# Kernel optimization log

Hardware: AMD Instinct MI355X
Metric: run time of the kernel (lower is better)

The kernel has to match this reference:

```python
import jax, jax.numpy as jnp
import numpy as np

T, B, IN, H, L, C = 512, 4096, 12, 32, 10, 4


def setup_inputs() -> dict:
    key = jax.random.key(0)
    ks = jax.random.split(key, 12)
    s = 1.0 / np.sqrt(H)  # PyTorch GRU init scale ~ U(-1/sqrt(H), 1/sqrt(H))
    return {
        "x": jax.random.normal(ks[0], (T, B, IN), jnp.float32),
        "W_ih0": jax.random.normal(ks[1], (3 * H, IN), jnp.float32) * s,
        "W_hh0": jax.random.normal(ks[2], (3 * H, H), jnp.float32) * s,
        "b_ih0": jax.random.normal(ks[3], (3 * H,), jnp.float32) * s,
        "b_hh0": jax.random.normal(ks[4], (3 * H,), jnp.float32) * s,
        "W_ih": jax.random.normal(ks[5], (L - 1, 3 * H, H), jnp.float32) * s,
        "W_hh": jax.random.normal(ks[6], (L - 1, 3 * H, H), jnp.float32) * s,
        "b_ih": jax.random.normal(ks[7], (L - 1, 3 * H), jnp.float32) * s,
        "b_hh": jax.random.normal(ks[8], (L - 1, 3 * H), jnp.float32) * s,
        "fc_W": jax.random.normal(ks[9], (C, H), jnp.float32) * s,
        "fc_b": jax.random.normal(ks[10], (C,), jnp.float32) * s,
        "lengths": jax.random.randint(ks[11], (B,), 1, T + 1, jnp.int32),
    }


def gru_cell(x_t, h, Wi, Wh, bi, bh):
    # PyTorch GRU cell math
    gi = x_t @ Wi.T + bi          # [B, 3H]
    gh = h @ Wh.T + bh            # [B, 3H]
    i_r, i_z, i_n = jnp.split(gi, 3, axis=-1)
    h_r, h_z, h_n = jnp.split(gh, 3, axis=-1)
    r = jax.nn.sigmoid(i_r + h_r)
    z = jax.nn.sigmoid(i_z + h_z)
    n = jnp.tanh(i_n + r * h_n)
    return (1.0 - z) * n + z * h


def reference(x, W_ih0, W_hh0, b_ih0, b_hh0, W_ih, W_hh, b_ih, b_hh, fc_W, fc_b, lengths):
    Bn = x.shape[1]
    h0 = jnp.zeros((L, Bn, H), x.dtype)

    def step(h, x_t):
        hs = []
        inp = x_t
        for l in range(L):
            if l == 0:
                hl = gru_cell(inp, h[0], W_ih0, W_hh0, b_ih0, b_hh0)
            else:
                hl = gru_cell(inp, h[l], W_ih[l - 1], W_hh[l - 1], b_ih[l - 1], b_hh[l - 1])
            hs.append(hl)
            inp = hl
        return jnp.stack(hs), inp  # carry all-layer hidden, emit top-layer output

    _, outs = jax.lax.scan(step, h0, x)  # [T, B, H]
    idx = jnp.maximum(lengths, 1) - 1    # last valid timestep per sequence
    last = outs[idx, jnp.arange(Bn)]     # [B, H]
    logits = last @ fc_W.T + fc_b        # [B, C]
    return jax.nn.log_softmax(logits, axis=1)
```

## Files before the change

### kernel.cpp

```cpp
#include <hip/hip_runtime.h>
#include <math.h>

#define TT 512
#define BB 4096
#define IN_DIM 12
#define HH 32
#define LL 10
#define CC 4
#define NTH (LL * 64)

typedef _Float16 half8 __attribute__((ext_vector_type(8)));
typedef _Float16 half4 __attribute__((ext_vector_type(4)));
typedef float f32x4 __attribute__((ext_vector_type(4)));
typedef float f32x2 __attribute__((ext_vector_type(2)));

#define LOG2E 1.44269504088896340736f

#define H_HI 0
#define H_LO (LL * 8 * 512)
#define X_HI (H_LO + LL * 2 * 512)
#define LDS16_TOT (X_HI + 4 * 512)

#define MFMA_(A, B, C) C = __builtin_amdgcn_mfma_f32_16x16x32_f16(A, B, C, 0, 0, 0)

__global__ __launch_bounds__(NTH, 2)
void gru_fused_mfma(const float* __restrict__ x,
                    const float* __restrict__ Wih0,
                    const float* __restrict__ Whh0,
                    const float* __restrict__ bih0,
                    const float* __restrict__ bhh0,
                    const float* __restrict__ Wih,
                    const float* __restrict__ Whh,
                    const float* __restrict__ bih,
                    const float* __restrict__ bhh,
                    const int*   __restrict__ lengths,
                    float*       __restrict__ last)
{
    __shared__ __align__(16) _Float16 lds16[LDS16_TOT];
    __shared__ int flagS[LL];
    __shared__ int rflagS[LL];

    const int tid  = threadIdx.x;
    const int w    = tid >> 6;
    const int lane = tid & 63;
    const int bi16 = lane & 15;
    const int quad = lane >> 4;
    const int bg   = blockIdx.x;

    {
        float4 z4 = make_float4(0.f, 0.f, 0.f, 0.f);
        float4* p = (float4*)lds16;
        for (int i = tid; i < LDS16_TOT / 8; i += NTH) p[i] = z4;
    }
    if (lane == 0) { flagS[w] = -1; rflagS[w] = -1; }
    __syncthreads();

    const float *Wi, *Wh, *bivec, *bhvec;
    int wistride;
    if (w == 0) { Wi = Wih0; Wh = Whh0; bivec = bih0; bhvec = bhh0; wistride = IN_DIM; }
    else {
        Wi = Wih + (size_t)(w - 1) * 96 * HH;
        Wh = Whh + (size_t)(w - 1) * 96 * HH;
        bivec = bih + (size_t)(w - 1) * 96;
        bhvec = bhh + (size_t)(w - 1) * 96;
        wistride = HH;
    }

    const int frow[12] = {0, 0, 16, 16, 32, 32, 48, 48, 64, 80, 64, 80};
    const int fchk[12] = {0, 1, 0, 1, 0, 1, 0, 1, 0, 0, 1, 1};
    half8 Whi[12], Wlo[6];
#pragma unroll
    for (int f = 0; f < 12; f++) {
        const float sc = (f < 8) ? -LOG2E : 2.0f * LOG2E;
        int row = frow[f] + bi16;
        const float* src; int kin;
        if (fchk[f] == 0) { src = Wi + (size_t)row * wistride; kin = wistride; }
        else              { src = Wh + (size_t)row * HH;       kin = HH; }
        int wloidx = (f < 8) ? (f >> 1) : (f - 6);
#pragma unroll
        for (int kk = 0; kk < 8; kk++) {
            int k = quad * 8 + kk;
            float v = (k < kin) ? src[k] * sc : 0.0f;
            _Float16 h = (_Float16)v;
            Whi[f][kk] = h;
            if (fchk[f] == 1) Wlo[wloidx][kk] = (_Float16)(v - (float)h);
        }
    }

    f32x4 biasreg[8];
#pragma unroll
    for (int ct = 0; ct < 8; ct++) {
        int g = ct >> 1, jt = ct & 1;
#pragma unroll
        for (int r = 0; r < 4; r++) {
            int j = jt * 16 + quad * 4 + r;
            float v;
            if      (g == 0) v = -(bivec[j]      + bhvec[j])      * LOG2E;
            else if (g == 1) v = -(bivec[32 + j] + bhvec[32 + j]) * LOG2E;
            else if (g == 2) v = bivec[64 + j] * (2.0f * LOG2E);
            else             v = bhvec[64 + j] * (2.0f * LOG2E);
            biasreg[ct][r] = v;
        }
    }

    int capT = -1;
    if (w == LL - 1) {
        int len = lengths[bg * 16 + bi16];
        capT = ((len < 1) ? 1 : len) - 1;
    }

    const int laneoff = lane * 8;
    const int inbase  = (w == 0) ? X_HI : (H_HI + (w - 1) * 4096);
    const int inmask  = (w == 0) ? 3 : 7;
    const int ownhi   = H_HI + w * 4096;
    const int ownlo   = H_LO + w * 1024;
    const int wibase  = (quad >> 1) * 128 + bi16 * 8 + (quad & 1) * 4;

    const int xbb = lane / 3, xkg = lane - xbb * 3;
    const int xq   = (xkg == 2) ? 1 : 0;
    const int xoff = (xkg == 1) ? 4 : 0;
    const int xidx = xq * 128 + xbb * 8 + xoff;
    const bool xlane = (w == 0) && (lane < 48);

    auto stage_x = [&](const float4& xl, int t) {
        half4 h4;
        h4[0] = (_Float16)xl.x; h4[1] = (_Float16)xl.y;
        h4[2] = (_Float16)xl.z; h4[3] = (_Float16)xl.w;
        *(half4*)(lds16 + X_HI + ((t & 3) << 9) + xidx) = h4;
    };

    if (xlane) {
        float4 x0 = *(const float4*)(x + (size_t)bg * 192 + lane * 4);
        float4 x1 = *(const float4*)(x + (size_t)BB * IN_DIM + (size_t)bg * 192 + lane * 4);
        stage_x(x0, 0);
        stage_x(x1, 1);
    }

    f32x2 hprev[4];
#pragma unroll
    for (int i = 0; i < 4; i++) { hprev[i][0] = 0.0f; hprev[i][1] = 0.0f; }

    __syncthreads();

    auto substep = [&](int t) {
        half8 bxh = *(const half8*)(lds16 + inbase + ((t & inmask) << 9) + laneoff);
        half8 bhh = *(const half8*)(lds16 + ownhi + (((t + 7) & 7) << 9) + laneoff);
        half8 bhl = *(const half8*)(lds16 + ownlo + (((t + 1) & 1) << 9) + laneoff);

        f32x4 acc[8];

#pragma unroll
        for (int ct = 0; ct < 4; ct++) {
            acc[ct] = __builtin_amdgcn_mfma_f32_16x16x32_f16(
                          Whi[ct * 2 + 0], bxh, biasreg[ct], 0, 0, 0);
            MFMA_(Whi[ct * 2 + 1], bhh, acc[ct]);
            MFMA_(Whi[ct * 2 + 1], bhl, acc[ct]);
            MFMA_(Wlo[ct],         bhh, acc[ct]);
        }
#pragma unroll
        for (int jt = 0; jt < 2; jt++) {
            acc[4 + jt] = __builtin_amdgcn_mfma_f32_16x16x32_f16(
                              Whi[8 + jt], bxh, biasreg[4 + jt], 0, 0, 0);
            acc[6 + jt] = __builtin_amdgcn_mfma_f32_16x16x32_f16(
                              Whi[10 + jt], bhh, biasreg[6 + jt], 0, 0, 0);
            MFMA_(Whi[10 + jt], bhl, acc[6 + jt]);
            MFMA_(Wlo[4 + jt],  bhh, acc[6 + jt]);
        }

#pragma unroll
        for (int jt = 0; jt < 2; jt++) {
            half4 h4, l4;
            float hv[4];
#pragma unroll
            for (int pr = 0; pr < 2; pr++) {
                f32x2 R2, Z2, I2, H2;
                R2[0] = acc[0 + jt][2 * pr]; R2[1] = acc[0 + jt][2 * pr + 1];
                Z2[0] = acc[2 + jt][2 * pr]; Z2[1] = acc[2 + jt][2 * pr + 1];
                I2[0] = acc[4 + jt][2 * pr]; I2[1] = acc[4 + jt][2 * pr + 1];
                H2[0] = acc[6 + jt][2 * pr]; H2[1] = acc[6 + jt][2 * pr + 1];
                f32x2 av, bv;
                av[0] = __builtin_amdgcn_exp2f(R2[0]);
                av[1] = __builtin_amdgcn_exp2f(R2[1]);
                bv[0] = __builtin_amdgcn_exp2f(Z2[0]);
                bv[1] = __builtin_amdgcn_exp2f(Z2[1]);
                av = av + 1.0f;
                bv = bv + 1.0f;
                f32x2 pv = av * bv;
                float q  = __builtin_amdgcn_rcpf(pv[0] * pv[1]);
                f32x2 qs; qs[0] = q * pv[1]; qs[1] = q * pv[0];
                f32x2 rv = qs * bv;
                f32x2 zv = qs * av;
                f32x2 na = __builtin_elementwise_fma(rv, H2, I2);
                f32x2 ea;
                ea[0] = __builtin_amdgcn_exp2f(na[0]);
                ea[1] = __builtin_amdgcn_exp2f(na[1]);
                f32x2 dv = ea + 1.0f;
                float qn = __builtin_amdgcn_rcpf(dv[0] * dv[1]);
                f32x2 qv; qv[0] = qn * dv[1]; qv[1] = qn * dv[0];
                f32x2 m2; m2[0] = -2.0f; m2[1] = -2.0f;
                f32x2 o1; o1[0] = 1.0f;  o1[1] = 1.0f;
                f32x2 nv = __builtin_elementwise_fma(m2, qv, o1);
                f32x2 hp = hprev[jt * 2 + pr];
                f32x2 hn = __builtin_elementwise_fma(zv, hp - nv, nv);
                hprev[jt * 2 + pr] = hn;
                _Float16 hh0 = (_Float16)hn[0], hh1 = (_Float16)hn[1];
                f32x2 hi32; hi32[0] = (float)hh0; hi32[1] = (float)hh1;
                f32x2 lo2 = hn - hi32;
                h4[2 * pr]     = hh0; h4[2 * pr + 1] = hh1;
                l4[2 * pr]     = (_Float16)lo2[0];
                l4[2 * pr + 1] = (_Float16)lo2[1];
                hv[2 * pr]     = hn[0];
                hv[2 * pr + 1] = hn[1];
            }
            int wi = jt * 256 + wibase;
            *(half4*)(lds16 + ownhi + ((t & 7) << 9) + wi) = h4;
            *(half4*)(lds16 + ownlo + ((t & 1) << 9) + wi) = l4;
            if (w == LL - 1 && t == capT) {
                float4 o = make_float4(hv[0], hv[1], hv[2], hv[3]);
                *(float4*)(last + (size_t)(bg * 16 + bi16) * HH + jt * 16 + quad * 4) = o;
            }
        }
    };

    for (int t = 0; t < TT; t += 2) {
        if (w > 0) {
            while (__hip_atomic_load(&flagS[w - 1], __ATOMIC_ACQUIRE,
                                     __HIP_MEMORY_SCOPE_WORKGROUP) < t + 1)
                __builtin_amdgcn_s_sleep(1);
        }
        if (w < LL - 1) {
            while (__hip_atomic_load(&rflagS[w], __ATOMIC_ACQUIRE,
                                     __HIP_MEMORY_SCOPE_WORKGROUP) < t - 7)
                __builtin_amdgcn_s_sleep(1);
        }

        float4 xa0, xa1;
        bool dl0 = false, dl1 = false;
        if (xlane) {
            if (t + 2 < TT) {
                xa0 = *(const float4*)(x + (size_t)(t + 2) * BB * IN_DIM +
                                       (size_t)bg * 192 + lane * 4);
                dl0 = true;
            }
            if (t + 3 < TT) {
                xa1 = *(const float4*)(x + (size_t)(t + 3) * BB * IN_DIM +
                                       (size_t)bg * 192 + lane * 4);
                dl1 = true;
            }
        }

        substep(t);
        substep(t + 1);

        if (dl0) stage_x(xa0, t + 2);
        if (dl1) stage_x(xa1, t + 3);

        if (lane == 0) {
            if (w < LL - 1)
                __hip_atomic_store(&flagS[w], t + 1, __ATOMIC_RELEASE,
                                   __HIP_MEMORY_SCOPE_WORKGROUP);
            if (w > 0)
                __hip_atomic_store(&rflagS[w - 1], t + 1, __ATOMIC_RELEASE,
                                   __HIP_MEMORY_SCOPE_WORKGROUP);
        }
    }
}

__global__ __launch_bounds__(256)
void fc_head(const float* __restrict__ last,
             const float* __restrict__ fcW,
             const float* __restrict__ fcb,
             float* __restrict__ out)
{
    int b = blockIdx.x * blockDim.x + threadIdx.x;
    if (b >= BB) return;
    float lg[CC];
#pragma unroll
    for (int c = 0; c < CC; c++) lg[c] = fcb[c];
#pragma unroll
    for (int j = 0; j < HH; j++) {
        float h = last[(size_t)b * HH + j];
#pragma unroll
        for (int c = 0; c < CC; c++) lg[c] = fmaf(fcW[c * HH + j], h, lg[c]);
    }
    float m = lg[0];
#pragma unroll
    for (int c = 1; c < CC; c++) m = fmaxf(m, lg[c]);
    float s = 0.0f;
#pragma unroll
    for (int c = 0; c < CC; c++) s += __expf(lg[c] - m);
    float lse = m + logf(s);
#pragma unroll
    for (int c = 0; c < CC; c++) out[(size_t)b * CC + c] = lg[c] - lse;
}

extern "C" void kernel_launch(void* const* d_in, const int* in_sizes, int n_in,
                              void* d_out, int out_size, void* d_ws, size_t ws_size,
                              hipStream_t stream)
{
    const float* x    = (const float*)d_in[0];
    const float* Wih0 = (const float*)d_in[1];
    const float* Whh0 = (const float*)d_in[2];
    const float* bih0 = (const float*)d_in[3];
    const float* bhh0 = (const float*)d_in[4];
    const float* Wih  = (const float*)d_in[5];
    const float* Whh  = (const float*)d_in[6];
    const float* bih  = (const float*)d_in[7];
    const float* bhh  = (const float*)d_in[8];
    const float* fcW  = (const float*)d_in[9];
    const float* fcb  = (const float*)d_in[10];
    const int*   lens = (const int*)d_in[11];
    float* out = (float*)d_out;

    float* last = (float*)d_ws;

    gru_fused_mfma<<<dim3(BB / 16), dim3(NTH), 0, stream>>>(
        x, Wih0, Whh0, bih0, bhh0, Wih, Whh, bih, bhh, lens, last);

    fc_head<<<dim3(BB / 256), dim3(256), 0, stream>>>(last, fcW, fcb, out);
}
```

Baseline: 908.7 us.

## Split last two GRU layers across two waves each to shorten pipeline critical path

Raises the block from 10 to 12 waves. Layers 8 and 9 are now each handled by two waves, and each wave of a pair computes one half (jt tile) of the hidden units. The sibling waves sync every substep through a new sibF flag array, and the forward and backward flag dependencies are rewired for the split layers. The intent is to speed up the slowest tail stages of the layer wavefront pipeline, at the cost of more waves per block (which can lower occupancy) and extra per-substep spin-waits.

```diff
diff --git a/kernel.cpp b/kernel.cpp
--- a/kernel.cpp
+++ b/kernel.cpp
@@ -7,7 +7,7 @@
 #define HH 32
 #define LL 10
 #define CC 4
-#define NTH (LL * 64)
+#define NTH 768
 
 typedef _Float16 half8 __attribute__((ext_vector_type(8)));
 typedef _Float16 half4 __attribute__((ext_vector_type(4)));
@@ -37,8 +37,9 @@
                     float*       __restrict__ last)
 {
     __shared__ __align__(16) _Float16 lds16[LDS16_TOT];
-    __shared__ int flagS[LL];
-    __shared__ int rflagS[LL];
+    __shared__ int flagS[12];
+    __shared__ int rflagS[12];
+    __shared__ int sibF[4];
 
     const int tid  = threadIdx.x;
     const int w    = tid >> 6;
@@ -47,22 +48,27 @@
     const int quad = lane >> 4;
     const int bg   = blockIdx.x;
 
+    const int  layer  = (w < 8) ? w : ((w < 10) ? 8 : 9);
+    const bool isHalf = (w >= 8);
+    const int  myjt   = (w < 8) ? 0 : ((w < 10) ? (w - 8) : (w - 10));
+
     {
         float4 z4 = make_float4(0.f, 0.f, 0.f, 0.f);
         float4* p = (float4*)lds16;
         for (int i = tid; i < LDS16_TOT / 8; i += NTH) p[i] = z4;
     }
     if (lane == 0) { flagS[w] = -1; rflagS[w] = -1; }
+    if (tid < 4) sibF[tid] = -1;
     __syncthreads();
 
     const float *Wi, *Wh, *bivec, *bhvec;
     int wistride;
-    if (w == 0) { Wi = Wih0; Wh = Whh0; bivec = bih0; bhvec = bhh0; wistride = IN_DIM; }
+    if (layer == 0) { Wi = Wih0; Wh = Whh0; bivec = bih0; bhvec = bhh0; wistride = IN_DIM; }
     else {
-        Wi = Wih + (size_t)(w - 1) * 96 * HH;
-        Wh = Whh + (size_t)(w - 1) * 96 * HH;
-        bivec = bih + (size_t)(w - 1) * 96;
-        bhvec = bhh + (size_t)(w - 1) * 96;
+        Wi = Wih + (size_t)(layer - 1) * 96 * HH;
+        Wh = Whh + (size_t)(layer - 1) * 96 * HH;
+        bivec = bih + (size_t)(layer - 1) * 96;
+        bhvec = bhh + (size_t)(layer - 1) * 96;
         wistride = HH;
     }
 
@@ -104,16 +110,16 @@
     }
 
     int capT = -1;
-    if (w == LL - 1) {
+    if (w >= 10) {
         int len = lengths[bg * 16 + bi16];
         capT = ((len < 1) ? 1 : len) - 1;
     }
 
     const int laneoff = lane * 8;
-    const int inbase  = (w == 0) ? X_HI : (H_HI + (w - 1) * 4096);
-    const int inmask  = (w == 0) ? 3 : 7;
-    const int ownhi   = H_HI + w * 4096;
-    const int ownlo   = H_LO + w * 1024;
+    const int inbase  = (layer == 0) ? X_HI : (H_HI + (layer - 1) * 4096);
+    const int inmask  = (layer == 0) ? 3 : 7;
+    const int ownhi   = H_HI + layer * 4096;
+    const int ownlo   = H_LO + layer * 1024;
     const int wibase  = (quad >> 1) * 128 + bi16 * 8 + (quad & 1) * 4;
 
     const int xbb = lane / 3, xkg = lane - xbb * 3;
@@ -143,6 +149,12 @@
     __syncthreads();
 
     auto substep = [&](int t) {
+        if (isHalf) {
+            while (__hip_atomic_load(&sibF[(w ^ 1) - 8], __ATOMIC_ACQUIRE,
+                                     __HIP_MEMORY_SCOPE_WORKGROUP) < t - 1)
+                __builtin_amdgcn_s_sleep(1);
+        }
+
         half8 bxh = *(const half8*)(lds16 + inbase + ((t & inmask) << 9) + laneoff);
         half8 bhh = *(const half8*)(lds16 + ownhi + (((t + 7) & 7) << 9) + laneoff);
         half8 bhl = *(const half8*)(lds16 + ownlo + (((t + 1) & 1) << 9) + laneoff);
@@ -151,24 +163,29 @@
 
 #pragma unroll
         for (int ct = 0; ct < 4; ct++) {
-            acc[ct] = __builtin_amdgcn_mfma_f32_16x16x32_f16(
-                          Whi[ct * 2 + 0], bxh, biasreg[ct], 0, 0, 0);
-            MFMA_(Whi[ct * 2 + 1], bhh, acc[ct]);
-            MFMA_(Whi[ct * 2 + 1], bhl, acc[ct]);
-            MFMA_(Wlo[ct],         bhh, acc[ct]);
+            if (!isHalf || (ct & 1) == myjt) {
+                acc[ct] = __builtin_amdgcn_mfma_f32_16x16x32_f16(
+                              Whi[ct * 2 + 0], bxh, biasreg[ct], 0, 0, 0);
+                MFMA_(Whi[ct * 2 + 1], bhh, acc[ct]);
+                MFMA_(Whi[ct * 2 + 1], bhl, acc[ct]);
+                MFMA_(Wlo[ct],         bhh, acc[ct]);
+            }
         }
 #pragma unroll
         for (int jt = 0; jt < 2; jt++) {
-            acc[4 + jt] = __builtin_amdgcn_mfma_f32_16x16x32_f16(
-                              Whi[8 + jt], bxh, biasreg[4 + jt], 0, 0, 0);
-            acc[6 + jt] = __builtin_amdgcn_mfma_f32_16x16x32_f16(
-                              Whi[10 + jt], bhh, biasreg[6 + jt], 0, 0, 0);
-            MFMA_(Whi[10 + jt], bhl, acc[6 + jt]);
-            MFMA_(Wlo[4 + jt],  bhh, acc[6 + jt]);
+            if (!isHalf || jt == myjt) {
+                acc[4 + jt] = __builtin_amdgcn_mfma_f32_16x16x32_f16(
+                                  Whi[8 + jt], bxh, biasreg[4 + jt], 0, 0, 0);
+                acc[6 + jt] = __builtin_amdgcn_mfma_f32_16x16x32_f16(
+                                  Whi[10 + jt], bhh, biasreg[6 + jt], 0, 0, 0);
+                MFMA_(Whi[10 + jt], bhl, acc[6 + jt]);
+                MFMA_(Wlo[4 + jt],  bhh, acc[6 + jt]);
+            }
         }
 
 #pragma unroll
         for (int jt = 0; jt < 2; jt++) {
+            if (isHalf && jt != myjt) continue;
             half4 h4, l4;
             float hv[4];
 #pragma unroll
@@ -215,21 +232,51 @@
             int wi = jt * 256 + wibase;
             *(half4*)(lds16 + ownhi + ((t & 7) << 9) + wi) = h4;
             *(half4*)(lds16 + ownlo + ((t & 1) << 9) + wi) = l4;
-            if (w == LL - 1 && t == capT) {
+            if (w >= 10 && t == capT) {
                 float4 o = make_float4(hv[0], hv[1], hv[2], hv[3]);
                 *(float4*)(last + (size_t)(bg * 16 + bi16) * HH + jt * 16 + quad * 4) = o;
             }
         }
+
+        if (isHalf && lane == 0) {
+            __hip_atomic_store(&sibF[w - 8], t, __ATOMIC_RELEASE,
+                               __HIP_MEMORY_SCOPE_WORKGROUP);
+        }
     };
 
     for (int t = 0; t < TT; t += 2) {
-        if (w > 0) {
+        if (w >= 1 && w <= 7) {
             while (__hip_atomic_load(&flagS[w - 1], __ATOMIC_ACQUIRE,
                                      __HIP_MEMORY_SCOPE_WORKGROUP) < t + 1)
                 __builtin_amdgcn_s_sleep(1);
-        }
-        if (w < LL - 1) {
-            while (__hip_atomic_load(&rflagS[w], __ATOMIC_ACQUIRE,
+        } else if (w == 8 || w == 9) {
+            while (__hip_atomic_load(&flagS[7], __ATOMIC_ACQUIRE,
+                                     __HIP_MEMORY_SCOPE_WORKGROUP) < t + 1)
+                __builtin_amdgcn_s_sleep(1);
+        } else if (w >= 10) {
+            while (__hip_atomic_load(&flagS[8], __ATOMIC_ACQUIRE,
+                                     __HIP_MEMORY_SCOPE_WORKGROUP) < t + 1)
+                __builtin_amdgcn_s_sleep(1);
+            while (__hip_atomic_load(&flagS[9], __ATOMIC_ACQUIRE,
+                                     __HIP_MEMORY_SCOPE_WORKGROUP) < t + 1)
+                __builtin_amdgcn_s_sleep(1);
+        }
+        if (w <= 6) {
+            while (__hip_atomic_load(&rflagS[w + 1], __ATOMIC_ACQUIRE,
+                                     __HIP_MEMORY_SCOPE_WORKGROUP) < t - 7)
+                __builtin_amdgcn_s_sleep(1);
+        } else if (w == 7) {
+            while (__hip_atomic_load(&rflagS[8], __ATOMIC_ACQUIRE,
+                                     __HIP_MEMORY_SCOPE_WORKGROUP) < t - 7)
+                __builtin_amdgcn_s_sleep(1);
+            while (__hip_atomic_load(&rflagS[9], __ATOMIC_ACQUIRE,
+                                     __HIP_MEMORY_SCOPE_WORKGROUP) < t - 7)
+                __builtin_amdgcn_s_sleep(1);
+        } else if (w == 8 || w == 9) {
+            while (__hip_atomic_load(&rflagS[10], __ATOMIC_ACQUIRE,
+                                     __HIP_MEMORY_SCOPE_WORKGROUP) < t - 7)
+                __builtin_amdgcn_s_sleep(1);
+            while (__hip_atomic_load(&rflagS[11], __ATOMIC_ACQUIRE,
                                      __HIP_MEMORY_SCOPE_WORKGROUP) < t - 7)
                 __builtin_amdgcn_s_sleep(1);
         }
@@ -256,11 +303,11 @@
         if (dl1) stage_x(xa1, t + 3);
 
         if (lane == 0) {
-            if (w < LL - 1)
+            if (w <= 9)
                 __hip_atomic_store(&flagS[w], t + 1, __ATOMIC_RELEASE,
                                    __HIP_MEMORY_SCOPE_WORKGROUP);
-            if (w > 0)
-                __hip_atomic_store(&rflagS[w - 1], t + 1, __ATOMIC_RELEASE,
+            if (w >= 1)
+                __hip_atomic_store(&rflagS[w], t + 1, __ATOMIC_RELEASE,
                                    __HIP_MEMORY_SCOPE_WORKGROUP);
         }
     }
```

After: 1.406 ms. 1.55x slower.

## Fuse FC head into GRU kernel and unroll time loop by eight

Applied to the files above, without the earlier changes.

The separate fc_head kernel is removed. The last hidden state is now captured in shared memory and the logits plus log-softmax are computed in-kernel by wave 0 using lane shuffles, which drops a launch and a global round trip. The time loop is also unrolled four pairs per iteration, so ring-buffer slot indices become compile-time constants and LDS address arithmetic is hoisted. The cost is a small extra LDS allocation, a final __syncthreads, and larger code.

```diff
diff --git a/kernel.cpp b/kernel.cpp
--- a/kernel.cpp
+++ b/kernel.cpp
@@ -34,9 +34,12 @@
                     const float* __restrict__ bih,
                     const float* __restrict__ bhh,
                     const int*   __restrict__ lengths,
-                    float*       __restrict__ last)
+                    const float* __restrict__ fcW,
+                    const float* __restrict__ fcb,
+                    float*       __restrict__ out)
 {
     __shared__ __align__(16) _Float16 lds16[LDS16_TOT];
+    __shared__ float lastF[16 * 33];
     __shared__ int flagS[LL];
     __shared__ int rflagS[LL];
 
@@ -112,9 +115,13 @@
     const int laneoff = lane * 8;
     const int inbase  = (w == 0) ? X_HI : (H_HI + (w - 1) * 4096);
     const int inmask  = (w == 0) ? 3 : 7;
-    const int ownhi   = H_HI + w * 4096;
-    const int ownlo   = H_LO + w * 1024;
     const int wibase  = (quad >> 1) * 128 + bi16 * 8 + (quad & 1) * 4;
+
+    const int inA   = inbase + laneoff;
+    const int hiR   = H_HI + w * 4096 + laneoff;
+    const int loR   = H_LO + w * 1024 + laneoff;
+    const int hiW   = H_HI + w * 4096 + wibase;
+    const int loW   = H_LO + w * 1024 + wibase;
 
     const int xbb = lane / 3, xkg = lane - xbb * 3;
     const int xq   = (xkg == 2) ? 1 : 0;
@@ -122,11 +129,11 @@
     const int xidx = xq * 128 + xbb * 8 + xoff;
     const bool xlane = (w == 0) && (lane < 48);
 
-    auto stage_x = [&](const float4& xl, int t) {
+    auto stage_x = [&](const float4& xl, int slot) {
         half4 h4;
         h4[0] = (_Float16)xl.x; h4[1] = (_Float16)xl.y;
         h4[2] = (_Float16)xl.z; h4[3] = (_Float16)xl.w;
-        *(half4*)(lds16 + X_HI + ((t & 3) << 9) + xidx) = h4;
+        *(half4*)(lds16 + X_HI + (slot << 9) + xidx) = h4;
     };
 
     if (xlane) {
@@ -142,10 +149,10 @@
 
     __syncthreads();
 
-    auto substep = [&](int t) {
-        half8 bxh = *(const half8*)(lds16 + inbase + ((t & inmask) << 9) + laneoff);
-        half8 bhh = *(const half8*)(lds16 + ownhi + (((t + 7) & 7) << 9) + laneoff);
-        half8 bhl = *(const half8*)(lds16 + ownlo + (((t + 1) & 1) << 9) + laneoff);
+    auto substep = [&](int t, int k) {
+        half8 bxh = *(const half8*)(lds16 + inA + ((k & inmask) << 9));
+        half8 bhh = *(const half8*)(lds16 + hiR + (((k + 7) & 7) << 9));
+        half8 bhl = *(const half8*)(lds16 + loR + (((k + 1) & 1) << 9));
 
         f32x4 acc[8];
 
@@ -212,86 +219,82 @@
                 hv[2 * pr]     = hn[0];
                 hv[2 * pr + 1] = hn[1];
             }
-            int wi = jt * 256 + wibase;
-            *(half4*)(lds16 + ownhi + ((t & 7) << 9) + wi) = h4;
-            *(half4*)(lds16 + ownlo + ((t & 1) << 9) + wi) = l4;
+            *(half4*)(lds16 + hiW + ((k & 7) << 9) + jt * 256) = h4;
+            *(half4*)(lds16 + loW + ((k & 1) << 9) + jt * 256) = l4;
             if (w == LL - 1 && t == capT) {
-                float4 o = make_float4(hv[0], hv[1], hv[2], hv[3]);
-                *(float4*)(last + (size_t)(bg * 16 + bi16) * HH + jt * 16 + quad * 4) = o;
+                lastF[bi16 * 33 + jt * 16 + quad * 4 + 0] = hv[0];
+                lastF[bi16 * 33 + jt * 16 + quad * 4 + 1] = hv[1];
+                lastF[bi16 * 33 + jt * 16 + quad * 4 + 2] = hv[2];
+                lastF[bi16 * 33 + jt * 16 + quad * 4 + 3] = hv[3];
             }
         }
     };
 
-    for (int t = 0; t < TT; t += 2) {
-        if (w > 0) {
-            while (__hip_atomic_load(&flagS[w - 1], __ATOMIC_ACQUIRE,
-                                     __HIP_MEMORY_SCOPE_WORKGROUP) < t + 1)
-                __builtin_amdgcn_s_sleep(1);
-        }
-        if (w < LL - 1) {
-            while (__hip_atomic_load(&rflagS[w], __ATOMIC_ACQUIRE,
-                                     __HIP_MEMORY_SCOPE_WORKGROUP) < t - 7)
-                __builtin_amdgcn_s_sleep(1);
-        }
-
-        float4 xa0, xa1;
-        bool dl0 = false, dl1 = false;
-        if (xlane) {
-            if (t + 2 < TT) {
-                xa0 = *(const float4*)(x + (size_t)(t + 2) * BB * IN_DIM +
-                                       (size_t)bg * 192 + lane * 4);
-                dl0 = true;
-            }
-            if (t + 3 < TT) {
-                xa1 = *(const float4*)(x + (size_t)(t + 3) * BB * IN_DIM +
-                                       (size_t)bg * 192 + lane * 4);
-                dl1 = true;
-            }
-        }
-
-        substep(t);
-        substep(t + 1);
-
-        if (dl0) stage_x(xa0, t + 2);
-        if (dl1) stage_x(xa1, t + 3);
-
-        if (lane == 0) {
-            if (w < LL - 1)
-                __hip_atomic_store(&flagS[w], t + 1, __ATOMIC_RELEASE,
-                                   __HIP_MEMORY_SCOPE_WORKGROUP);
-            if (w > 0)
-                __hip_atomic_store(&rflagS[w - 1], t + 1, __ATOMIC_RELEASE,
-                                   __HIP_MEMORY_SCOPE_WORKGROUP);
-        }
-    }
-}
-
-__global__ __launch_bounds__(256)
-void fc_head(const float* __restrict__ last,
-             const float* __restrict__ fcW,
-             const float* __restrict__ fcb,
-             float* __restrict__ out)
-{
-    int b = blockIdx.x * blockDim.x + threadIdx.x;
-    if (b >= BB) return;
-    float lg[CC];
-#pragma unroll
-    for (int c = 0; c < CC; c++) lg[c] = fcb[c];
-#pragma unroll
-    for (int j = 0; j < HH; j++) {
-        float h = last[(size_t)b * HH + j];
-#pragma unroll
-        for (int c = 0; c < CC; c++) lg[c] = fmaf(fcW[c * HH + j], h, lg[c]);
-    }
-    float m = lg[0];
-#pragma unroll
-    for (int c = 1; c < CC; c++) m = fmaxf(m, lg[c]);
-    float s = 0.0f;
-#pragma unroll
-    for (int c = 0; c < CC; c++) s += __expf(lg[c] - m);
-    float lse = m + logf(s);
-#pragma unroll
-    for (int c = 0; c < CC; c++) out[(size_t)b * CC + c] = lg[c] - lse;
+#define PAIR(kp)                                                          \
+    do {                                                                  \
+        const int t = tb + (kp);                                          \
+        if (w > 0) {                                                      \
+            while (__hip_atomic_load(&flagS[w - 1], __ATOMIC_ACQUIRE,     \
+                                     __HIP_MEMORY_SCOPE_WORKGROUP) < t + 1)\
+                __builtin_amdgcn_s_sleep(1);                              \
+        }                                                                 \
+        if (w < LL - 1) {                                                 \
+            while (__hip_atomic_load(&rflagS[w], __ATOMIC_ACQUIRE,        \
+                                     __HIP_MEMORY_SCOPE_WORKGROUP) < t - 7)\
+                __builtin_amdgcn_s_sleep(1);                              \
+        }                                                                 \
+        float4 xa0, xa1;                                                  \
+        bool dl0 = false, dl1 = false;                                    \
+        if (xlane) {                                                      \
+            if (t + 2 < TT) {                                             \
+                xa0 = *(const float4*)(x + (size_t)(t + 2) * BB * IN_DIM +\
+                                       (size_t)bg * 192 + lane * 4);      \
+                dl0 = true;                                               \
+            }                                                             \
+            if (t + 3 < TT) {                                             \
+                xa1 = *(const float4*)(x + (size_t)(t + 3) * BB * IN_DIM +\
+                                       (size_t)bg * 192 + lane * 4);      \
+                dl1 = true;                                               \
+            }                                                             \
+        }                                                                 \
+        substep(t, (kp));                                                 \
+        substep(t + 1, (kp) + 1);                                         \
+        if (dl0) stage_x(xa0, ((kp) + 2) & 3);                            \
+        if (dl1) stage_x(xa1, ((kp) + 3) & 3);                            \
+        if (lane == 0) {                                                  \
+            if (w < LL - 1)                                               \
+                __hip_atomic_store(&flagS[w], t + 1, __ATOMIC_RELEASE,    \
+                                   __HIP_MEMORY_SCOPE_WORKGROUP);         \
+            if (w > 0)                                                    \
+                __hip_atomic_store(&rflagS[w - 1], t + 1, __ATOMIC_RELEASE,\
+                                   __HIP_MEMORY_SCOPE_WORKGROUP);         \
+        }                                                                 \
+    } while (0)
+
+    for (int tb = 0; tb < TT; tb += 8) {
+        PAIR(0);
+        PAIR(2);
+        PAIR(4);
+        PAIR(6);
+    }
+#undef PAIR
+
+    __syncthreads();
+    if (w == 0) {
+        const int b = lane & 15;
+        const int c = lane >> 4;
+        float lg = fcb[c];
+#pragma unroll
+        for (int j = 0; j < HH; j++)
+            lg = fmaf(fcW[c * HH + j], lastF[b * 33 + j], lg);
+        float m = fmaxf(lg, __shfl_xor(lg, 16));
+        m = fmaxf(m, __shfl_xor(m, 32));
+        float e = __expf(lg - m);
+        float s = e + __shfl_xor(e, 16);
+        s += __shfl_xor(s, 32);
+        float lse = m + logf(s);
+        out[(size_t)(bg * 16 + b) * CC + c] = lg - lse;
+    }
 }
 
 extern "C" void kernel_launch(void* const* d_in, const int* in_sizes, int n_in,
@@ -312,10 +315,6 @@
     const int*   lens = (const int*)d_in[11];
     float* out = (float*)d_out;
 
-    float* last = (float*)d_ws;
-
     gru_fused_mfma<<<dim3(BB / 16), dim3(NTH), 0, stream>>>(
-        x, Wih0, Whh0, bih0, bhh0, Wih, Whh, bih, bhh, lens, last);
-
-    fc_head<<<dim3(BB / 256), dim3(256), 0, stream>>>(last, fcW, fcb, out);
+        x, Wih0, Whh0, bih0, bhh0, Wih, Whh, bih, bhh, lens, fcW, fcb, out);
 }
```

Result: slower. 949.5 us (+4.5%).
